# Kernel tuning notes

Hardware: AMD Instinct MI355X
Metric: run time of the kernel (lower is better)

The kernel has to match this reference:

```python
import jax, jax.numpy as jnp
import numpy as np

G, B, DEG, BATCH = 4000, 8, 32, 128  # genes, per-gene layersize, off-diag blocks/gene, batch


def setup_inputs() -> dict:
    key = jax.random.key(0)
    rng = np.random.default_rng(0)
    # block structure: DEG off-diagonal PPI blocks per gene + reflexive diagonal
    src = np.repeat(np.arange(G, dtype=np.int32), DEG)
    off = 1 + rng.integers(0, G - 1, size=G * DEG)          # never 0 -> off-diagonal
    dst = ((src.astype(np.int64) + off) % G).astype(np.int32)
    diag = np.arange(G, dtype=np.int32)
    block_in = jnp.asarray(np.concatenate([src, diag]))      # [N] = [G*DEG + G]
    block_out = jnp.asarray(np.concatenate([dst, diag]))     # [N]
    n_blocks = G * DEG + G
    k1, k2 = jax.random.split(key)
    x = jax.random.normal(k1, (BATCH, G * B), dtype=jnp.float32)
    w = jax.random.normal(k2, (n_blocks, B, B), dtype=jnp.float32) * 0.05
    return {"x": x, "w": w, "block_in": block_in, "block_out": block_out}


def reference(x, w, block_in, block_out):
    batch, d = x.shape
    n_blocks, b, _ = w.shape
    g = d // b
    xb = x.reshape(batch, g, b)
    xin = xb[:, block_in, :]                        # [batch, N, b] irregular gather
    contrib = jnp.einsum('bni,nio->nbo', xin, w)    # [N, batch, b] tiny per-block GEMMs
    out = jax.ops.segment_sum(contrib, block_out, num_segments=g)  # [g, batch, b] scatter-add
    out = jnp.transpose(out, (1, 0, 2)).reshape(batch, d)
    # activation_function is identity (default lambda x: x); residual=True
    return out + x
```

## Files before the change

kernel.cpp:

```cpp
#include <hip/hip_runtime.h>
#include <hip/hip_bf16.h>

#define G      4000
#define DEG    32
#define BATCH  128
#define D      32000
#define NBLK   132000
#define ZBLK   NBLK
#define CAP    96
#define SCAP   112

typedef __attribute__((ext_vector_type(8))) short bf16x8;
typedef __attribute__((ext_vector_type(4))) float f32x4;

__device__ inline unsigned bf16rne(float f) {
    unsigned u = __float_as_uint(f);
    return (u + 0x7fffu + ((u >> 16) & 1u)) >> 16;
}

__global__ void zero_cnt_kernel(int* cnt) {
    int i = blockIdx.x * 256 + threadIdx.x;
    if (i < G) cnt[i] = 0;
}

#define NB_BUILD 516
#define NB_TR    1000
#define NB_W     2063

__global__ __launch_bounds__(256) void prep_kernel(const float* __restrict__ x,
                                                   const float* __restrict__ w,
                                                   const int* __restrict__ block_in,
                                                   const int* __restrict__ block_out,
                                                   int* __restrict__ cnt,
                                                   int2* __restrict__ pairs,
                                                   unsigned short* __restrict__ xgb,
                                                   unsigned short* __restrict__ wtb) {
    __shared__ float shmem[64 * 68];
    const int bid = blockIdx.x;
    const int t   = threadIdx.x;

    if (bid < NB_BUILD) {
        int n = bid * 256 + t;
        if (n < NBLK) {
            int dst = block_out[n];
            int src = block_in[n];
            int pos = atomicAdd(&cnt[dst], 1);
            if (pos < CAP) pairs[dst * CAP + pos] = make_int2(n, src);
        }
    } else if (bid < NB_BUILD + NB_TR) {
        int id = bid - NB_BUILD;
        int c0 = (id % 250) * 128;
        int b0 = (id / 250) * 32;
        int half = (b0 >= 64) ? 1 : 0;
        int lr0  = b0 & 63;
#pragma unroll
        for (int it = 0; it < 4; ++it) {
            int l  = it * 1024 + t * 4;
            int br = l >> 7;
            int c  = l & 127;
            float4 v = *(const float4*)(x + (size_t)(b0 + br) * D + c0 + c);
            *(float4*)&shmem[br * 132 + c] = v;
        }
        __syncthreads();
#pragma unroll
        for (int it = 0; it < 2; ++it) {
            int idx = it * 256 + t;
            int gl  = idx >> 5;
            int bl  = idx & 31;
            float4 v0 = *(const float4*)&shmem[bl * 132 + gl * 8];
            float4 v1 = *(const float4*)&shmem[bl * 132 + gl * 8 + 4];
            uint4 p;
            p.x = bf16rne(v0.x) | (bf16rne(v0.y) << 16);
            p.y = bf16rne(v0.z) | (bf16rne(v0.w) << 16);
            p.z = bf16rne(v1.x) | (bf16rne(v1.y) << 16);
            p.w = bf16rne(v1.z) | (bf16rne(v1.w) << 16);
            int gidx = (c0 >> 3) + gl;
            size_t base = (((size_t)half * G + gidx) * 64 + lr0 + bl) * 8;
            *(uint4*)(xgb + base) = p;
        }
    } else {
        int    id       = bid - (NB_BUILD + NB_TR);
        size_t base_blk = (size_t)id * 64;
        const float* wb = w + base_blk * 64;
#pragma unroll
        for (int j = 0; j < 4; ++j) {
            int pos  = j * 1024 + t * 4;
            int nl   = pos >> 6;
            int rest = pos & 63;
            float4 v;
            if (base_blk + nl < NBLK) v = *(const float4*)(wb + pos);
            else                      v = make_float4(0.f, 0.f, 0.f, 0.f);
            *(float4*)&shmem[nl * 68 + rest] = v;
        }
        __syncthreads();
#pragma unroll
        for (int j = 0; j < 2; ++j) {
            int p  = j * 256 + t;
            int nl = p >> 3;
            int o  = p & 7;
            size_t nglob = base_blk + nl;
            if (nglob <= NBLK) {
                const float* r = &shmem[nl * 68 + o];
                uint4 q;
                q.x = bf16rne(r[0])  | (bf16rne(r[8])  << 16);
                q.y = bf16rne(r[16]) | (bf16rne(r[24]) << 16);
                q.z = bf16rne(r[32]) | (bf16rne(r[40]) << 16);
                q.w = bf16rne(r[48]) | (bf16rne(r[56]) << 16);
                *(uint4*)(wtb + nglob * 64 + o * 8) = q;
            }
        }
    }
}

__global__ __launch_bounds__(128) void compute_kernel(const float* __restrict__ x,
                                                      const unsigned short* __restrict__ xgb,
                                                      const unsigned short* __restrict__ wtb,
                                                      const int2* __restrict__ pairs,
                                                      const int* __restrict__ cnt,
                                                      float* __restrict__ out) {
    const int blk  = blockIdx.x;
    const int xcd8 = blk & 7;
    const int half = xcd8 >> 2;
    const int g    = (blk >> 3) * 4 + (blk & 3);
    const int t    = threadIdx.x;
    const int wave = t >> 6;
    const int lane = t & 63;
    const int quad = lane >> 4;
    const int lo16 = lane & 15;

    __shared__ int2 se[SCAP];

    const int col  = g * 8 + lo16;
    const int row0 = half * 64 + wave * 32 + quad * 4;
    float rx0[4], rx1[4];
    if (lo16 < 8) {
#pragma unroll
        for (int r = 0; r < 4; ++r) {
            rx0[r] = x[(size_t)(row0 + r) * D + col];
            rx1[r] = x[(size_t)(row0 + 16 + r) * D + col];
        }
    }

    int m = cnt[g];
    if (m > CAP) m = CAP;
    if (t < SCAP) {
        int2 e = (t < m) ? pairs[(size_t)g * CAP + t] : make_int2(ZBLK, 0);
        se[t] = e;
    }
    __syncthreads();

    const int ob    = lo16 & 7;
    const int bboff = ob * 8;
    const int mt0   = wave * 32 + lo16;
    const int a0off = mt0 * 8;
    const int a1off = a0off + 128;
    const size_t hbase = (size_t)half * G;

    f32x4 acc0 = {0.f, 0.f, 0.f, 0.f};
    f32x4 acc1 = {0.f, 0.f, 0.f, 0.f};

#define LOADAB(k0, A0, A1, BB)                                            \
    do {                                                                  \
        int2 e_ = se[(k0) + quad];                                        \
        const unsigned short* xb_ = xgb + ((hbase + e_.y) << 9);          \
        A0 = *(const uint4*)(xb_ + a0off);                                \
        A1 = *(const uint4*)(xb_ + a1off);                                \
        BB = *(const uint4*)(wtb + (((size_t)e_.x) << 6) + bboff);        \
    } while (0)

#define CONS(A0, A1, BB)                                                  \
    do {                                                                  \
        acc0 = __builtin_amdgcn_mfma_f32_16x16x32_bf16(                   \
            __builtin_bit_cast(bf16x8, A0), __builtin_bit_cast(bf16x8, BB), acc0, 0, 0, 0); \
        acc1 = __builtin_amdgcn_mfma_f32_16x16x32_bf16(                   \
            __builtin_bit_cast(bf16x8, A1), __builtin_bit_cast(bf16x8, BB), acc1, 0, 0, 0); \
    } while (0)

    uint4 Pa0, Pa1, Pb, Qa0, Qa1, Qb;

    LOADAB(0, Pa0, Pa1, Pb);
    LOADAB(4, Qa0, Qa1, Qb);

    for (int k0 = 0; k0 + 8 < m; k0 += 8) {
        CONS(Pa0, Pa1, Pb);
        LOADAB(k0 + 8, Pa0, Pa1, Pb);
        CONS(Qa0, Qa1, Qb);
        LOADAB(k0 + 12, Qa0, Qa1, Qb);
    }
    CONS(Pa0, Pa1, Pb);
    CONS(Qa0, Qa1, Qb);

    if (lo16 < 8) {
#pragma unroll
        for (int r = 0; r < 4; ++r) {
            out[(size_t)(row0 + r) * D + col]      = acc0[r] + rx0[r];
            out[(size_t)(row0 + 16 + r) * D + col] = acc1[r] + rx1[r];
        }
    }
#undef LOADAB
#undef CONS
}

extern "C" void kernel_launch(void* const* d_in, const int* in_sizes, int n_in,
                              void* d_out, int out_size, void* d_ws, size_t ws_size,
                              hipStream_t stream) {
    const float* x         = (const float*)d_in[0];
    const float* w         = (const float*)d_in[1];
    const int*   block_in  = (const int*)d_in[2];
    const int*   block_out = (const int*)d_in[3];
    float*       out       = (float*)d_out;

    char* ws = (char*)d_ws;
    int*            cnt   = (int*)ws;
    int2*           pairs = (int2*)(ws + 16384);
    unsigned short* xgb   = (unsigned short*)(ws + 3088384);
    unsigned short* wtb   = (unsigned short*)(ws + 11280384);

    zero_cnt_kernel<<<16, 256, 0, stream>>>(cnt);
    prep_kernel<<<NB_BUILD + NB_TR + NB_W, 256, 0, stream>>>(x, w, block_in, block_out,
                                                             cnt, pairs, xgb, wtb);
    compute_kernel<<<G * 2, 128, 0, stream>>>(x, xgb, wtb, pairs, cnt, out);
}
```

Measured before the change: 143.0 us.

## Convert weights to bf16 inside compute kernel instead of separate prep pass

Removes the weight transpose and bf16 conversion stage from the prep kernel. The compute kernel now reads fp32 weights directly with strided scalar loads and converts them to bf16 in registers. A zero pad buffer stands in for the padding block. This avoids writing and re-reading a converted weight copy, but each of the two half-batch blocks now reads fp32 weights (twice the bytes) with eight strided scalar loads per lane instead of one 16-byte load.

```diff
diff --git a/kernel.cpp b/kernel.cpp
--- a/kernel.cpp
+++ b/kernel.cpp
@@ -18,24 +18,22 @@
     return (u + 0x7fffu + ((u >> 16) & 1u)) >> 16;
 }
 
-__global__ void zero_cnt_kernel(int* cnt) {
+__global__ void zero_cnt_kernel(int* cnt, float* zpad) {
     int i = blockIdx.x * 256 + threadIdx.x;
     if (i < G) cnt[i] = 0;
+    if (i < 64) zpad[i] = 0.f;
 }
 
 #define NB_BUILD 516
 #define NB_TR    1000
-#define NB_W     2063
 
 __global__ __launch_bounds__(256) void prep_kernel(const float* __restrict__ x,
-                                                   const float* __restrict__ w,
                                                    const int* __restrict__ block_in,
                                                    const int* __restrict__ block_out,
                                                    int* __restrict__ cnt,
                                                    int2* __restrict__ pairs,
-                                                   unsigned short* __restrict__ xgb,
-                                                   unsigned short* __restrict__ wtb) {
-    __shared__ float shmem[64 * 68];
+                                                   unsigned short* __restrict__ xgb) {
+    __shared__ float shmem[32 * 132];
     const int bid = blockIdx.x;
     const int t   = threadIdx.x;
 
@@ -47,7 +45,7 @@
             int pos = atomicAdd(&cnt[dst], 1);
             if (pos < CAP) pairs[dst * CAP + pos] = make_int2(n, src);
         }
-    } else if (bid < NB_BUILD + NB_TR) {
+    } else {
         int id = bid - NB_BUILD;
         int c0 = (id % 250) * 128;
         int b0 = (id / 250) * 32;
@@ -78,43 +76,13 @@
             size_t base = (((size_t)half * G + gidx) * 64 + lr0 + bl) * 8;
             *(uint4*)(xgb + base) = p;
         }
-    } else {
-        int    id       = bid - (NB_BUILD + NB_TR);
-        size_t base_blk = (size_t)id * 64;
-        const float* wb = w + base_blk * 64;
-#pragma unroll
-        for (int j = 0; j < 4; ++j) {
-            int pos  = j * 1024 + t * 4;
-            int nl   = pos >> 6;
-            int rest = pos & 63;
-            float4 v;
-            if (base_blk + nl < NBLK) v = *(const float4*)(wb + pos);
-            else                      v = make_float4(0.f, 0.f, 0.f, 0.f);
-            *(float4*)&shmem[nl * 68 + rest] = v;
-        }
-        __syncthreads();
-#pragma unroll
-        for (int j = 0; j < 2; ++j) {
-            int p  = j * 256 + t;
-            int nl = p >> 3;
-            int o  = p & 7;
-            size_t nglob = base_blk + nl;
-            if (nglob <= NBLK) {
-                const float* r = &shmem[nl * 68 + o];
-                uint4 q;
-                q.x = bf16rne(r[0])  | (bf16rne(r[8])  << 16);
-                q.y = bf16rne(r[16]) | (bf16rne(r[24]) << 16);
-                q.z = bf16rne(r[32]) | (bf16rne(r[40]) << 16);
-                q.w = bf16rne(r[48]) | (bf16rne(r[56]) << 16);
-                *(uint4*)(wtb + nglob * 64 + o * 8) = q;
-            }
-        }
     }
 }
 
 __global__ __launch_bounds__(128) void compute_kernel(const float* __restrict__ x,
                                                       const unsigned short* __restrict__ xgb,
-                                                      const unsigned short* __restrict__ wtb,
+                                                      const float* __restrict__ wsrc,
+                                                      const float* __restrict__ zpad,
                                                       const int2* __restrict__ pairs,
                                                       const int* __restrict__ cnt,
                                                       float* __restrict__ out) {
@@ -150,7 +118,7 @@
     __syncthreads();
 
     const int ob    = lo16 & 7;
-    const int bboff = ob * 8;
+    const float* zp = zpad + ob;
     const int mt0   = wave * 32 + lo16;
     const int a0off = mt0 * 8;
     const int a1off = a0off + 128;
@@ -165,7 +133,13 @@
         const unsigned short* xb_ = xgb + ((hbase + e_.y) << 9);          \
         A0 = *(const uint4*)(xb_ + a0off);                                \
         A1 = *(const uint4*)(xb_ + a1off);                                \
-        BB = *(const uint4*)(wtb + (((size_t)e_.x) << 6) + bboff);        \
+        const float* wp_ = (e_.x != ZBLK) ? (wsrc + (((size_t)e_.x) << 6) + ob) : zp; \
+        float f0_ = wp_[0],  f1_ = wp_[8],  f2_ = wp_[16], f3_ = wp_[24]; \
+        float f4_ = wp_[32], f5_ = wp_[40], f6_ = wp_[48], f7_ = wp_[56]; \
+        BB.x = bf16rne(f0_) | (bf16rne(f1_) << 16);                       \
+        BB.y = bf16rne(f2_) | (bf16rne(f3_) << 16);                       \
+        BB.z = bf16rne(f4_) | (bf16rne(f5_) << 16);                       \
+        BB.w = bf16rne(f6_) | (bf16rne(f7_) << 16);                       \
     } while (0)
 
 #define CONS(A0, A1, BB)                                                  \
@@ -214,10 +188,10 @@
     int*            cnt   = (int*)ws;
     int2*           pairs = (int2*)(ws + 16384);
     unsigned short* xgb   = (unsigned short*)(ws + 3088384);
-    unsigned short* wtb   = (unsigned short*)(ws + 11280384);
+    float*          zpad  = (float*)(ws + 11280384);
 
-    zero_cnt_kernel<<<16, 256, 0, stream>>>(cnt);
-    prep_kernel<<<NB_BUILD + NB_TR + NB_W, 256, 0, stream>>>(x, w, block_in, block_out,
-                                                             cnt, pairs, xgb, wtb);
-    compute_kernel<<<G * 2, 128, 0, stream>>>(x, xgb, wtb, pairs, cnt, out);
+    zero_cnt_kernel<<<16, 256, 0, stream>>>(cnt, zpad);
+    prep_kernel<<<NB_BUILD + NB_TR, 256, 0, stream>>>(x, block_in, block_out,
+                                                      cnt, pairs, xgb);
+    compute_kernel<<<G * 2, 128, 0, stream>>>(x, xgb, w, zpad, pairs, cnt, out);
 }
```

Result: faster. 140.0 us (-2.1%).
